# Kernel optimization log

Hardware: AMD Instinct MI355X
Metric: run time of the kernel (lower is better)

The kernel has to match this reference:

```python
import jax, jax.numpy as jnp
import numpy as np

B, C, D, W, H = 4, 256, 32, 32, 32  # img_dim = D, in_channels = C, model_num = 4


def setup_inputs() -> dict:
    key = jax.random.key(0)
    ks = jax.random.split(key, 8)
    s = 0.02
    inp = {
        "m1": jax.random.normal(ks[0], (B, C, D, W, H), jnp.float32),
        "m2": jax.random.normal(ks[1], (B, C, D, W, H), jnp.float32),
        "m3": jax.random.normal(ks[2], (B, C, D, W, H), jnp.float32),
        "m4": jax.random.normal(ks[3], (B, C, D, W, H), jnp.float32),
        # nn.Linear weights (torch convention: y = x @ W.T + b)
        "Wq": jax.random.normal(ks[4], (D, D), jnp.float32) * s,
        "bq": jnp.zeros((D,), jnp.float32),
        "Wk": jax.random.normal(ks[5], (D, D), jnp.float32) * s,
        "bk": jnp.zeros((D,), jnp.float32),
        # four 1x1x1 Conv3d kernels, squeezed to [model, out_c, in_c]
        "Wc": jax.random.normal(ks[6], (4, C, C), jnp.float32) * s,
        "bc": jnp.zeros((4, C), jnp.float32),
    }
    return inp


def reference(m1, m2, m3, m4, Wq, bq, Wk, bk, Wc, bc):
    d = m1.shape[2]
    # adaptive_avg_pool3d(x, (D,1,1)) == mean over W,H -> [B,C,D]; stack 4 modalities -> [B,C,4,D]
    pooled = jnp.stack([m.mean(axis=(3, 4)) for m in (m1, m2, m3, m4)], axis=2)
    q = jnp.einsum('bcd,ed->bce', pooled[:, :, 0], Wq) + bq          # [B,C,D]
    k = jnp.einsum('bcmd,ed->bcme', pooled, Wk) + bk                 # [B,C,4,D]
    # per-modality attention logits: q . k_m over D -> [B,C,4]
    a = jnp.einsum('bcd,bcmd->bcm', q, k) / jnp.sqrt(jnp.float32(d))
    a = jax.nn.softmax(a, axis=-1)                                   # [B,C,4]
    ms = jnp.stack([m1, m2, m3, m4], axis=0)                         # [4,B,C,D,W,H]
    # 1x1x1 Conv3d == channel-mixing GEMM per voxel
    conv = jnp.einsum('mbcdwh,moc->mbodwh', ms, Wc) + bc[:, None, :, None, None, None]
    # weighted sum of the 4 conv outputs by per-(B,C) attention weights
    out = jnp.einsum('bcm,mbcdwh->bcdwh', a, conv)                   # [B,C,D,W,H]
    return out
```

## Files before the change

### kernel.cpp

```cpp
#include <hip/hip_runtime.h>
#include <hip/hip_bf16.h>

#define NB 4
#define NC 256
#define ND 32
#define WH 1024
#define DWH 32768
#define KTOT 1024

typedef __attribute__((ext_vector_type(8))) short short8;
typedef __attribute__((ext_vector_type(4))) float f32x4;

static __device__ __forceinline__ unsigned short f32_to_bf16(float f) {
    unsigned u = __builtin_bit_cast(unsigned, f);
    u = u + 0x7fff + ((u >> 16) & 1);
    return (unsigned short)(u >> 16);
}

static __device__ __forceinline__ unsigned pack_bf16x2(float lo, float hi) {
    __hip_bfloat162 h = __float22bfloat162_rn(make_float2(lo, hi));
    unsigned u;
    __builtin_memcpy(&u, &h, 4);
    return u;
}

__global__ __launch_bounds__(256) void transpool_kernel(
    const float* __restrict__ i0, const float* __restrict__ i1,
    const float* __restrict__ i2, const float* __restrict__ i3,
    unsigned short* __restrict__ Bt, float* __restrict__ pooled)
{
    __shared__ float lds[64 * 132];
    int bid = blockIdx.x;
    int d  = bid & 31;
    int cb = (bid >> 5) & 3;
    int m  = (bid >> 7) & 3;
    int b  = bid >> 9;
    const float* base = (m == 0 ? i0 : m == 1 ? i1 : m == 2 ? i2 : i3)
                        + ((size_t)(b * NC + cb * 64)) * DWH + d * WH;
    int t  = threadIdx.x;
    int rl = t >> 3;
    int xo = t & 7;
    int xr = t >> 1;
    int ch = t & 1;

    float pc0 = 0.f, pc1 = 0.f;
    float4 v0[4], v1[4];

    #pragma unroll
    for (int j = 0; j < 4; ++j) {
        v0[j] = *(const float4*)(base + (size_t)rl * DWH + (xo + 8 * j) * 4);
        v1[j] = *(const float4*)(base + (size_t)(32 + rl) * DWH + (xo + 8 * j) * 4);
    }
    #pragma unroll
    for (int j = 0; j < 4; ++j) {
        pc0 += v0[j].x + v0[j].y + v0[j].z + v0[j].w;
        pc1 += v1[j].x + v1[j].y + v1[j].z + v1[j].w;
        *(float4*)&lds[rl * 132 + (xo + 8 * j) * 4]        = v0[j];
        *(float4*)&lds[(32 + rl) * 132 + (xo + 8 * j) * 4] = v1[j];
    }
    __syncthreads();

    unsigned short* tb0 = Bt + (((size_t)b * 256 + d * 8) * 16 + (m * 4 + cb)) * 8192;

    #pragma unroll 1
    for (int s = 0; s < 8; ++s) {
        if (s < 7) {
            const float* bs = base + (s + 1) * 128;
            #pragma unroll
            for (int j = 0; j < 4; ++j) {
                v0[j] = *(const float4*)(bs + (size_t)rl * DWH + (xo + 8 * j) * 4);
                v1[j] = *(const float4*)(bs + (size_t)(32 + rl) * DWH + (xo + 8 * j) * 4);
            }
        }
        {
            unsigned short* dst = tb0 + (size_t)s * 16 * 8192 + (size_t)xr * 64 + ch * 32;
            unsigned pk[16];
            #pragma unroll
            for (int i = 0; i < 16; ++i) {
                float f0 = lds[(ch * 32 + 2 * i) * 132 + xr];
                float f1 = lds[(ch * 32 + 2 * i + 1) * 132 + xr];
                pk[i] = pack_bf16x2(f0, f1);
            }
            #pragma unroll
            for (int u = 0; u < 4; ++u)
                *(uint4*)(dst + u * 8) =
                    (uint4){pk[4 * u], pk[4 * u + 1], pk[4 * u + 2], pk[4 * u + 3]};
        }
        __syncthreads();
        if (s < 7) {
            #pragma unroll
            for (int j = 0; j < 4; ++j) {
                pc0 += v0[j].x + v0[j].y + v0[j].z + v0[j].w;
                pc1 += v1[j].x + v1[j].y + v1[j].z + v1[j].w;
                *(float4*)&lds[rl * 132 + (xo + 8 * j) * 4]        = v0[j];
                *(float4*)&lds[(32 + rl) * 132 + (xo + 8 * j) * 4] = v1[j];
            }
            __syncthreads();
        }
    }

    pc0 += __shfl_down(pc0, 4, 64); pc1 += __shfl_down(pc1, 4, 64);
    pc0 += __shfl_down(pc0, 2, 64); pc1 += __shfl_down(pc1, 2, 64);
    pc0 += __shfl_down(pc0, 1, 64); pc1 += __shfl_down(pc1, 1, 64);
    if (xo == 0) {
        pooled[((size_t)b * NC + cb * 64 + rl) * 128 + m * 32 + d]      = pc0 * (1.0f / 1024.0f);
        pooled[((size_t)b * NC + cb * 64 + 32 + rl) * 128 + m * 32 + d] = pc1 * (1.0f / 1024.0f);
    }
}

__global__ __launch_bounds__(256) void pool_kernel(
    const float* __restrict__ i0, const float* __restrict__ i1,
    const float* __restrict__ i2, const float* __restrict__ i3,
    float* __restrict__ pooled)
{
    int bid = blockIdx.x;
    int m   = bid & 3;
    int bc  = bid >> 2;
    const float* src = (m == 0 ? i0 : m == 1 ? i1 : m == 2 ? i2 : i3)
                       + (size_t)bc * DWH;
    int t = threadIdx.x;
    int d   = t >> 3;
    int sub = t & 7;

    const float4* row = (const float4*)(src + (size_t)d * WH);
    float4 a0 = {0.f, 0.f, 0.f, 0.f}, a1 = {0.f, 0.f, 0.f, 0.f};
    #pragma unroll
    for (int j = 0; j < 16; ++j) {
        float4 u = row[sub + 8 * (2 * j)];
        float4 w = row[sub + 8 * (2 * j + 1)];
        a0.x += u.x; a0.y += u.y; a0.z += u.z; a0.w += u.w;
        a1.x += w.x; a1.y += w.y; a1.z += w.z; a1.w += w.w;
    }
    float s = (a0.x + a0.y) + (a0.z + a0.w) + (a1.x + a1.y) + (a1.z + a1.w);
    s += __shfl_down(s, 4, 64);
    s += __shfl_down(s, 2, 64);
    s += __shfl_down(s, 1, 64);
    if (sub == 0) pooled[bc * 128 + m * 32 + d] = s * (1.0f / 1024.0f);
}

__global__ __launch_bounds__(64) void attn_kernel(
    const float* __restrict__ pooled,
    const float* __restrict__ Wq, const float* __restrict__ bq,
    const float* __restrict__ Wk, const float* __restrict__ bk,
    const float* __restrict__ Wc, const float* __restrict__ bcv,
    unsigned short* __restrict__ Amat, float* __restrict__ beff)
{
    int bc_idx = blockIdx.x;
    int lane = threadIdx.x;
    int e = lane & 31;
    const float* P = pooled + bc_idx * 128;

    float q = 0.f, kv[4] = {0.f, 0.f, 0.f, 0.f};
    for (int d = 0; d < 32; ++d) {
        float pq = P[d];
        float wq = Wq[e * 32 + d], wk = Wk[e * 32 + d];
        q += pq * wq;
        #pragma unroll
        for (int m = 0; m < 4; ++m) kv[m] += P[m * 32 + d] * wk;
    }
    q += bq[e];
    #pragma unroll
    for (int m = 0; m < 4; ++m) kv[m] += bk[e];

    float lg[4];
    #pragma unroll
    for (int m = 0; m < 4; ++m) {
        float p = q * kv[m];
        #pragma unroll
        for (int off = 16; off; off >>= 1) p += __shfl_xor(p, off, 32);
        lg[m] = p * 0.17677669529663687f;
    }
    float mx = fmaxf(fmaxf(lg[0], lg[1]), fmaxf(lg[2], lg[3]));
    float ex[4], s = 0.f;
    #pragma unroll
    for (int m = 0; m < 4; ++m) { ex[m] = __expf(lg[m] - mx); s += ex[m]; }
    float a[4];
    #pragma unroll
    for (int m = 0; m < 4; ++m) a[m] = ex[m] / s;

    int c = bc_idx & 255;
    if (lane == 0) {
        float be = 0.f;
        #pragma unroll
        for (int m = 0; m < 4; ++m) be += a[m] * bcv[m * NC + c];
        beff[bc_idx] = be;
    }
    unsigned short* Arow = Amat + (size_t)bc_idx * KTOT;
    #pragma unroll
    for (int j = 0; j < 16; ++j) {
        int k = j * 64 + lane;
        int m = k >> 8, cin = k & 255;
        float v = a[m] * Wc[(m * NC + c) * NC + cin];
        Arow[k] = f32_to_bf16(v);
    }
}

#define BM 128
#define BN 128
#define BK 64

static __device__ __forceinline__ int swzA(int row, int chunk) {
    return row * 64 + ((chunk ^ (row & 7)) << 3);
}
static __device__ __forceinline__ int swzB(int row, int chunk) {
    return row * 64 + ((chunk ^ ((row >> 1) & 7)) << 3);
}

__global__ __launch_bounds__(256, 2) void gemm2_kernel(
    const unsigned short* __restrict__ Amat,
    const unsigned short* __restrict__ Bt,
    const float* __restrict__ beff,
    float* __restrict__ out)
{
    __shared__ __align__(16) short As[2 * BM * BK];
    __shared__ __align__(16) short Bs[2 * BN * BK];

    int raw = blockIdx.x;
    int sb  = (raw & 7) * 256 + (raw >> 3);
    int ot = sb & 1;
    int xt = (sb >> 1) & 255;
    int b  = sb >> 9;
    int o0 = ot * BM, x0 = xt * BN;

    int t = threadIdx.x;
    int wave = t >> 6, lane = t & 63;
    int wr = wave >> 1, wc = wave & 1;
    int lrow = lane & 15, lk = lane >> 4;
    int lr8 = lane >> 3;
    int aq  = (lane & 7) ^ lr8;

    const unsigned short* asrc = Amat + ((size_t)b * NC + o0) * KTOT
                                 + (size_t)(wave * 32 + lr8) * KTOT + aq * 8;
    const unsigned short* bsrc = Bt + ((size_t)b * 256 + xt) * 16 * 8192
                                 + (size_t)(wave * 32 + lr8) * 64 + aq * 8;

    f32x4 acc[4][4];
    #pragma unroll
    for (int mi = 0; mi < 4; ++mi)
        #pragma unroll
        for (int ni = 0; ni < 4; ++ni)
            acc[mi][ni] = (f32x4){0.f, 0.f, 0.f, 0.f};

    #pragma unroll
    for (int p = 0; p < 4; ++p)
        __builtin_amdgcn_global_load_lds(
            (const __attribute__((address_space(1))) unsigned int*)
                (asrc + (size_t)p * 8 * KTOT),
            (__attribute__((address_space(3))) unsigned int*)
                (As + (wave * 32 + p * 8) * 64), 16, 0, 0);
    #pragma unroll
    for (int p = 0; p < 4; ++p)
        __builtin_amdgcn_global_load_lds(
            (const __attribute__((address_space(1))) unsigned int*)
                (bsrc + (size_t)p * 8 * 64),
            (__attribute__((address_space(3))) unsigned int*)
                (Bs + (wave * 32 + p * 8) * 64), 16, 0, 0);
    __builtin_amdgcn_sched_barrier(0);

    #pragma unroll 1
    for (int it = 0; it < 16; ++it) {
        int ja = (it < 15) ? it + 1 : 15;
        int bo = ((it + 1) & 1) * (BM * BK);
        #pragma unroll
        for (int p = 0; p < 4; ++p)
            __builtin_amdgcn_global_load_lds(
                (const __attribute__((address_space(1))) unsigned int*)
                    (asrc + (size_t)p * 8 * KTOT + ja * BK),
                (__attribute__((address_space(3))) unsigned int*)
                    (As + bo + (wave * 32 + p * 8) * 64), 16, 0, 0);
        #pragma unroll
        for (int p = 0; p < 4; ++p)
            __builtin_amdgcn_global_load_lds(
                (const __attribute__((address_space(1))) unsigned int*)
                    (bsrc + (size_t)ja * 8192 + p * 8 * 64),
                (__attribute__((address_space(3))) unsigned int*)
                    (Bs + bo + (wave * 32 + p * 8) * 64), 16, 0, 0);
        __builtin_amdgcn_sched_barrier(0);

        asm volatile("s_waitcnt vmcnt(8)" ::: "memory");
        __builtin_amdgcn_s_barrier();
        __builtin_amdgcn_sched_barrier(0);

        const short* Acur = As + (it & 1) * (BM * BK);
        const short* Bcur = Bs + (it & 1) * (BM * BK);
        #pragma unroll
        for (int kk = 0; kk < 2; ++kk) {
            int q = kk * 4 + lk;
            short8 af[4], bf[4];
            #pragma unroll
            for (int mi = 0; mi < 4; ++mi)
                af[mi] = *(const short8*)(&Acur[swzA(wr * 64 + mi * 16 + lrow, q)]);
            #pragma unroll
            for (int ni = 0; ni < 4; ++ni)
                bf[ni] = *(const short8*)(&Bcur[swzA(wc * 64 + ni * 16 + lrow, q)]);
            __builtin_amdgcn_s_setprio(1);
            #pragma unroll
            for (int mi = 0; mi < 4; ++mi)
                #pragma unroll
                for (int ni = 0; ni < 4; ++ni)
                    acc[mi][ni] = __builtin_amdgcn_mfma_f32_16x16x32_bf16(
                        af[mi], bf[ni], acc[mi][ni], 0, 0, 0);
            __builtin_amdgcn_s_setprio(0);
        }
        __builtin_amdgcn_s_barrier();
        __builtin_amdgcn_sched_barrier(0);
    }

    const float* beff_b = beff + b * NC + o0;
    float* outb = out + ((size_t)b * NC + o0) * DWH + x0;
    #pragma unroll
    for (int mi = 0; mi < 4; ++mi) {
        #pragma unroll
        for (int r4 = 0; r4 < 4; ++r4) {
            int row = wr * 64 + mi * 16 + lk * 4 + r4;
            float bias = beff_b[row];
            float* orow = outb + (size_t)row * DWH;
            #pragma unroll
            for (int ni = 0; ni < 4; ++ni) {
                int col = wc * 64 + ni * 16 + lrow;
                orow[col] = acc[mi][ni][r4] + bias;
            }
        }
    }
}

__global__ __launch_bounds__(256, 3) void gemm_kernel(
    const float* __restrict__ i0, const float* __restrict__ i1,
    const float* __restrict__ i2, const float* __restrict__ i3,
    const unsigned short* __restrict__ Amat,
    const float* __restrict__ beff,
    float* __restrict__ out)
{
    __shared__ __align__(16) short As[2 * BM * BK];
    __shared__ __align__(16) short Bs[BN * BK];

    int raw = blockIdx.x;
    int sb  = (raw & 7) * 256 + (raw >> 3);
    int ot = sb & 1;
    int xt = (sb >> 1) & 255;
    int b  = sb >> 9;
    int o0 = ot * BM, x0 = xt * BN;

    const unsigned short* Ab = Amat + ((size_t)b * NC + o0) * KTOT;

    int t = threadIdx.x;
    int wave = t >> 6, lane = t & 63;
    int wr = wave >> 1, wc = wave & 1;
    int lrow = lane & 15, lk = lane >> 4;

    f32x4 acc[4][4];
    #pragma unroll
    for (int mi = 0; mi < 4; ++mi)
        #pragma unroll
        for (int ni = 0; ni < 4; ++ni)
            acc[mi][ni] = (f32x4){0.f, 0.f, 0.f, 0.f};

    int xq = t & 31;
    int kb = (t >> 5) * 8;

    int ar = wave * 32 + (lane >> 3);
    int aq = (lane & 7) ^ (lane >> 3);
    const unsigned short* asrc = Ab + (size_t)ar * KTOT + aq * 8;

    float4 v[8];

    {
        #pragma unroll
        for (int p = 0; p < 4; ++p)
            __builtin_amdgcn_global_load_lds(
                (const __attribute__((address_space(1))) unsigned int*)
                    (asrc + (size_t)p * 8 * KTOT),
                (__attribute__((address_space(3))) unsigned int*)
                    (As + (wave * 32 + p * 8) * 64), 16, 0, 0);
        const float* Bb = i0 + (size_t)b * NC * DWH + x0;
        #pragma unroll
        for (int j = 0; j < 8; ++j)
            v[j] = *(const float4*)(Bb + (size_t)(kb + j) * DWH + xq * 4);
    }

    #pragma unroll 1
    for (int it = 0; it < KTOT / BK; ++it) {
        const short* Acur = As + (it & 1) * (BM * BK);
        short* Anx = As + ((it + 1) & 1) * (BM * BK);

        __builtin_amdgcn_s_barrier();
        __builtin_amdgcn_sched_barrier(0);

        {
            int ja = (it + 1 < 16) ? it + 1 : 15;
            #pragma unroll
            for (int p = 0; p < 4; ++p)
                __builtin_amdgcn_global_load_lds(
                    (const __attribute__((address_space(1))) unsigned int*)
                        (asrc + (size_t)p * 8 * KTOT + ja * BK),
                    (__attribute__((address_space(3))) unsigned int*)
                        (Anx + (wave * 32 + p * 8) * 64), 16, 0, 0);
        }
        __builtin_amdgcn_sched_barrier(0);

        uint4 pk[4];
        #pragma unroll
        for (int i = 0; i < 4; ++i) {
            unsigned w[4];
            #pragma unroll
            for (int j = 0; j < 4; ++j)
                w[j] = pack_bf16x2(((const float*)&v[2 * j])[i],
                                   ((const float*)&v[2 * j + 1])[i]);
            pk[i] = (uint4){w[0], w[1], w[2], w[3]};
        }

        {
            int itn = (it < 15) ? it + 1 : 15;
            int m = itn >> 2, cbase = (itn & 3) * 64;
            const float* Bb = (m == 0 ? i0 : m == 1 ? i1 : m == 2 ? i2 : i3)
                              + ((size_t)b * NC + cbase) * DWH + x0;
            #pragma unroll
            for (int j = 0; j < 8; ++j)
                v[j] = *(const float4*)(Bb + (size_t)(kb + j) * DWH + xq * 4);
        }
        __builtin_amdgcn_sched_barrier(0);

        #pragma unroll
        for (int i = 0; i < 4; ++i)
            *(uint4*)(&Bs[swzB(xq * 4 + i, t >> 5)]) = pk[i];

        asm volatile("s_waitcnt vmcnt(12) lgkmcnt(0)" ::: "memory");
        __builtin_amdgcn_s_barrier();
        __builtin_amdgcn_sched_barrier(0);

        #pragma unroll
        for (int kk = 0; kk < 2; ++kk) {
            int q = kk * 4 + lk;
            short8 af[4], bf[4];
            #pragma unroll
            for (int mi = 0; mi < 4; ++mi)
                af[mi] = *(const short8*)(&Acur[swzA(wr * 64 + mi * 16 + lrow, q)]);
            #pragma unroll
            for (int ni = 0; ni < 4; ++ni)
                bf[ni] = *(const short8*)(&Bs[swzB(wc * 64 + ni * 16 + lrow, q)]);
            __builtin_amdgcn_s_setprio(1);
            #pragma unroll
            for (int mi = 0; mi < 4; ++mi)
                #pragma unroll
                for (int ni = 0; ni < 4; ++ni)
                    acc[mi][ni] = __builtin_amdgcn_mfma_f32_16x16x32_bf16(
                        af[mi], bf[ni], acc[mi][ni], 0, 0, 0);
            __builtin_amdgcn_s_setprio(0);
        }
    }

    const float* beff_b = beff + b * NC + o0;
    float* outb = out + ((size_t)b * NC + o0) * DWH + x0;
    #pragma unroll
    for (int mi = 0; mi < 4; ++mi) {
        #pragma unroll
        for (int r4 = 0; r4 < 4; ++r4) {
            int row = wr * 64 + mi * 16 + lk * 4 + r4;
            float bias = beff_b[row];
            float* orow = outb + (size_t)row * DWH;
            #pragma unroll
            for (int ni = 0; ni < 4; ++ni) {
                int col = wc * 64 + ni * 16 + lrow;
                orow[col] = acc[mi][ni][r4] + bias;
            }
        }
    }
}

extern "C" void kernel_launch(void* const* d_in, const int* in_sizes, int n_in,
                              void* d_out, int out_size, void* d_ws, size_t ws_size,
                              hipStream_t stream) {
    const float* m1 = (const float*)d_in[0];
    const float* m2 = (const float*)d_in[1];
    const float* m3 = (const float*)d_in[2];
    const float* m4 = (const float*)d_in[3];
    const float* Wq = (const float*)d_in[4];
    const float* bq = (const float*)d_in[5];
    const float* Wk = (const float*)d_in[6];
    const float* bk = (const float*)d_in[7];
    const float* Wc = (const float*)d_in[8];
    const float* bcv = (const float*)d_in[9];
    float* out = (float*)d_out;

    const size_t BT_BYTES = (size_t)NB * KTOT * DWH * 2;
    const size_t NEED = BT_BYTES + 524288 + 2097152 + 4096;

    if (ws_size >= NEED) {
        unsigned short* Btr   = (unsigned short*)d_ws;
        float* pooled         = (float*)((char*)d_ws + BT_BYTES);
        unsigned short* Amat  = (unsigned short*)((char*)d_ws + BT_BYTES + 524288);
        float* beff           = (float*)((char*)d_ws + BT_BYTES + 524288 + 2097152);

        transpool_kernel<<<2048, 256, 0, stream>>>(m1, m2, m3, m4, Btr, pooled);
        attn_kernel<<<NB * NC, 64, 0, stream>>>(pooled, Wq, bq, Wk, bk, Wc, bcv,
                                                Amat, beff);
        gemm2_kernel<<<2048, 256, 0, stream>>>(Amat, Btr, beff, out);
    } else {
        float* pooled        = (float*)d_ws;
        unsigned short* Amat = (unsigned short*)((char*)d_ws + 524288);
        float* beff          = (float*)((char*)d_ws + 524288 + 2097152);

        pool_kernel<<<NB * NC * 4, 256, 0, stream>>>(m1, m2, m3, m4, pooled);
        attn_kernel<<<NB * NC, 64, 0, stream>>>(pooled, Wq, bq, Wk, bk, Wc, bcv,
                                                Amat, beff);
        gemm_kernel<<<(NB) * (NC / BM) * (DWH / BN), 256, 0, stream>>>(
            m1, m2, m3, m4, Amat, beff, out);
    }
}
```

Measured before the change: 305.9 us.

## Double-buffer register loads and rework LDS transpose layout in transpool kernel

The transpose+pool kernel now keeps two register buffers of input tiles, so loads for step s+2 are in flight while step s is written out, instead of prefetching only one step ahead. The LDS row stride goes from 132 to 133 floats, and the store phase is remapped so each thread reads 8 consecutive channel rows and writes one 16-byte chunk per output row. Together these aim to hide global load latency and cut LDS bank conflicts. The cost is more registers per thread, which may lower occupancy, and scalar LDS writes where vector writes were used before.

Result: faster. 289.7 us (-5.3%).

```diff
diff --git a/kernel.cpp b/kernel.cpp
--- a/kernel.cpp
+++ b/kernel.cpp
@@ -24,12 +24,49 @@
     return u;
 }
 
+#define TP_LOAD(V, S)                                                         \
+  { const float* bs_ = base + (S) * 128;                                      \
+    _Pragma("unroll")                                                         \
+    for (int j_ = 0; j_ < 4; ++j_) {                                          \
+      V[j_]     = *(const float4*)(bs_ + (size_t)rl * DWH + (xo + 8 * j_) * 4);\
+      V[j_ + 4] = *(const float4*)(bs_ + (size_t)(32 + rl) * DWH + (xo + 8 * j_) * 4);\
+    } }
+
+#define TP_STAGE(V)                                                           \
+  { _Pragma("unroll")                                                         \
+    for (int j_ = 0; j_ < 4; ++j_) {                                          \
+      float4 u_ = V[j_], w_ = V[j_ + 4];                                      \
+      pc0 += u_.x + u_.y + u_.z + u_.w;                                       \
+      pc1 += w_.x + w_.y + w_.z + w_.w;                                       \
+      int xb_ = (xo + 8 * j_) * 4;                                            \
+      lds[rl * 133 + xb_ + 0] = u_.x;  lds[rl * 133 + xb_ + 1] = u_.y;        \
+      lds[rl * 133 + xb_ + 2] = u_.z;  lds[rl * 133 + xb_ + 3] = u_.w;        \
+      lds[(32 + rl) * 133 + xb_ + 0] = w_.x;  lds[(32 + rl) * 133 + xb_ + 1] = w_.y;\
+      lds[(32 + rl) * 133 + xb_ + 2] = w_.z;  lds[(32 + rl) * 133 + xb_ + 3] = w_.w;\
+    } }
+
+#define TP_STORE(S)                                                           \
+  { unsigned short* tile_ = tb0 + (size_t)(S) * 16 * 8192;                    \
+    _Pragma("unroll")                                                         \
+    for (int u_ = 0; u_ < 4; ++u_) {                                          \
+      int row_ = u_ * 32 + rl;                                                \
+      unsigned w0_ = pack_bf16x2(lds[(8 * xo + 0) * 133 + row_],              \
+                                 lds[(8 * xo + 1) * 133 + row_]);             \
+      unsigned w1_ = pack_bf16x2(lds[(8 * xo + 2) * 133 + row_],              \
+                                 lds[(8 * xo + 3) * 133 + row_]);             \
+      unsigned w2_ = pack_bf16x2(lds[(8 * xo + 4) * 133 + row_],              \
+                                 lds[(8 * xo + 5) * 133 + row_]);             \
+      unsigned w3_ = pack_bf16x2(lds[(8 * xo + 6) * 133 + row_],              \
+                                 lds[(8 * xo + 7) * 133 + row_]);             \
+      *(uint4*)(tile_ + (size_t)row_ * 64 + xo * 8) = (uint4){w0_, w1_, w2_, w3_};\
+    } }
+
 __global__ __launch_bounds__(256) void transpool_kernel(
     const float* __restrict__ i0, const float* __restrict__ i1,
     const float* __restrict__ i2, const float* __restrict__ i3,
     unsigned short* __restrict__ Bt, float* __restrict__ pooled)
 {
-    __shared__ float lds[64 * 132];
+    __shared__ float lds[64 * 133];
     int bid = blockIdx.x;
     int d  = bid & 31;
     int cb = (bid >> 5) & 3;
@@ -40,61 +77,30 @@
     int t  = threadIdx.x;
     int rl = t >> 3;
     int xo = t & 7;
-    int xr = t >> 1;
-    int ch = t & 1;
 
     float pc0 = 0.f, pc1 = 0.f;
-    float4 v0[4], v1[4];
-
-    #pragma unroll
-    for (int j = 0; j < 4; ++j) {
-        v0[j] = *(const float4*)(base + (size_t)rl * DWH + (xo + 8 * j) * 4);
-        v1[j] = *(const float4*)(base + (size_t)(32 + rl) * DWH + (xo + 8 * j) * 4);
-    }
-    #pragma unroll
-    for (int j = 0; j < 4; ++j) {
-        pc0 += v0[j].x + v0[j].y + v0[j].z + v0[j].w;
-        pc1 += v1[j].x + v1[j].y + v1[j].z + v1[j].w;
-        *(float4*)&lds[rl * 132 + (xo + 8 * j) * 4]        = v0[j];
-        *(float4*)&lds[(32 + rl) * 132 + (xo + 8 * j) * 4] = v1[j];
-    }
+    float4 va[8], vb[8];
+
+    unsigned short* tb0 = Bt + (((size_t)b * 256 + d * 8) * 16 + (m * 4 + cb)) * 8192;
+
+    TP_LOAD(va, 0);
+    TP_LOAD(vb, 1);
+    TP_STAGE(va);
     __syncthreads();
 
-    unsigned short* tb0 = Bt + (((size_t)b * 256 + d * 8) * 16 + (m * 4 + cb)) * 8192;
-
     #pragma unroll 1
-    for (int s = 0; s < 8; ++s) {
-        if (s < 7) {
-            const float* bs = base + (s + 1) * 128;
-            #pragma unroll
-            for (int j = 0; j < 4; ++j) {
-                v0[j] = *(const float4*)(bs + (size_t)rl * DWH + (xo + 8 * j) * 4);
-                v1[j] = *(const float4*)(bs + (size_t)(32 + rl) * DWH + (xo + 8 * j) * 4);
-            }
-        }
-        {
-            unsigned short* dst = tb0 + (size_t)s * 16 * 8192 + (size_t)xr * 64 + ch * 32;
-            unsigned pk[16];
-            #pragma unroll
-            for (int i = 0; i < 16; ++i) {
-                float f0 = lds[(ch * 32 + 2 * i) * 132 + xr];
-                float f1 = lds[(ch * 32 + 2 * i + 1) * 132 + xr];
-                pk[i] = pack_bf16x2(f0, f1);
-            }
-            #pragma unroll
-            for (int u = 0; u < 4; ++u)
-                *(uint4*)(dst + u * 8) =
-                    (uint4){pk[4 * u], pk[4 * u + 1], pk[4 * u + 2], pk[4 * u + 3]};
-        }
+    for (int s2 = 0; s2 < 4; ++s2) {
+        int s = 2 * s2;
+        if (s2 < 3) TP_LOAD(va, s + 2);
+        TP_STORE(s);
         __syncthreads();
-        if (s < 7) {
-            #pragma unroll
-            for (int j = 0; j < 4; ++j) {
-                pc0 += v0[j].x + v0[j].y + v0[j].z + v0[j].w;
-                pc1 += v1[j].x + v1[j].y + v1[j].z + v1[j].w;
-                *(float4*)&lds[rl * 132 + (xo + 8 * j) * 4]        = v0[j];
-                *(float4*)&lds[(32 + rl) * 132 + (xo + 8 * j) * 4] = v1[j];
-            }
+        TP_STAGE(vb);
+        __syncthreads();
+        if (s2 < 3) TP_LOAD(vb, s + 3);
+        TP_STORE(s + 1);
+        __syncthreads();
+        if (s2 < 3) {
+            TP_STAGE(va);
             __syncthreads();
         }
     }
```

## Split transpose-pool kernel into small 8-channel blocks with XCD-aware block remap

Applied to the files above, without the earlier changes.

The fused transpose-and-pool kernel is restructured so that each block handles 8 channels by one depth slice in a single pass. Previously each block covered 64 channels and looped over 8 staging rounds. The grid grows from 2048 to 16384 blocks, and block ids are remapped by stride 8, apparently to spread work across the chip's compute dies. Each thread now writes 16-byte bf16 chunks that hold 8 channels, and the pooled mean uses a wider shuffle reduction. This aims to raise parallelism and remove the loop's per-round synchronization, at the cost of narrower 16-byte output writes scattered across memory and more blocks to launch.

Result: slower. 514.7 us (+68.3%).

```diff
diff --git a/kernel.cpp b/kernel.cpp
--- a/kernel.cpp
+++ b/kernel.cpp
@@ -29,82 +29,69 @@
     const float* __restrict__ i2, const float* __restrict__ i3,
     unsigned short* __restrict__ Bt, float* __restrict__ pooled)
 {
-    __shared__ float lds[64 * 132];
-    int bid = blockIdx.x;
-    int d  = bid & 31;
-    int cb = (bid >> 5) & 3;
-    int m  = (bid >> 7) & 3;
-    int b  = bid >> 9;
+    __shared__ float lds[8 * 1024];
+    int raw = blockIdx.x;
+    int sb  = (raw & 7) * 2048 + (raw >> 3);
+    int d    = sb & 31;
+    int cb8  = (sb >> 5) & 31;
+    int m    = (sb >> 10) & 3;
+    int b    = sb >> 12;
     const float* base = (m == 0 ? i0 : m == 1 ? i1 : m == 2 ? i2 : i3)
-                        + ((size_t)(b * NC + cb * 64)) * DWH + d * WH;
-    int t  = threadIdx.x;
-    int rl = t >> 3;
-    int xo = t & 7;
-    int xr = t >> 1;
-    int ch = t & 1;
-
-    float pc0 = 0.f, pc1 = 0.f;
-    float4 v0[4], v1[4];
-
-    #pragma unroll
-    for (int j = 0; j < 4; ++j) {
-        v0[j] = *(const float4*)(base + (size_t)rl * DWH + (xo + 8 * j) * 4);
-        v1[j] = *(const float4*)(base + (size_t)(32 + rl) * DWH + (xo + 8 * j) * 4);
-    }
-    #pragma unroll
-    for (int j = 0; j < 4; ++j) {
-        pc0 += v0[j].x + v0[j].y + v0[j].z + v0[j].w;
-        pc1 += v1[j].x + v1[j].y + v1[j].z + v1[j].w;
-        *(float4*)&lds[rl * 132 + (xo + 8 * j) * 4]        = v0[j];
-        *(float4*)&lds[(32 + rl) * 132 + (xo + 8 * j) * 4] = v1[j];
-    }
+                        + ((size_t)(b * NC + cb8 * 8)) * DWH + d * WH;
+
+    int t = threadIdx.x;
+    int row    = t >> 5;
+    int lane32 = t & 31;
+
+    float4 v[8];
+    #pragma unroll
+    for (int j = 0; j < 8; ++j)
+        v[j] = *(const float4*)(base + (size_t)row * DWH + lane32 * 4 + j * 128);
+
+    float s = 0.f;
+    #pragma unroll
+    for (int j = 0; j < 8; ++j)
+        s += (v[j].x + v[j].y) + (v[j].z + v[j].w);
+
+    #pragma unroll
+    for (int j = 0; j < 8; ++j)
+        *(float4*)&lds[row * 1024 + lane32 * 4 + j * 128] = v[j];
     __syncthreads();
 
-    unsigned short* tb0 = Bt + (((size_t)b * 256 + d * 8) * 16 + (m * 4 + cb)) * 8192;
-
-    #pragma unroll 1
-    for (int s = 0; s < 8; ++s) {
-        if (s < 7) {
-            const float* bs = base + (s + 1) * 128;
-            #pragma unroll
-            for (int j = 0; j < 4; ++j) {
-                v0[j] = *(const float4*)(bs + (size_t)rl * DWH + (xo + 8 * j) * 4);
-                v1[j] = *(const float4*)(bs + (size_t)(32 + rl) * DWH + (xo + 8 * j) * 4);
-            }
-        }
-        {
-            unsigned short* dst = tb0 + (size_t)s * 16 * 8192 + (size_t)xr * 64 + ch * 32;
-            unsigned pk[16];
-            #pragma unroll
-            for (int i = 0; i < 16; ++i) {
-                float f0 = lds[(ch * 32 + 2 * i) * 132 + xr];
-                float f1 = lds[(ch * 32 + 2 * i + 1) * 132 + xr];
-                pk[i] = pack_bf16x2(f0, f1);
-            }
-            #pragma unroll
-            for (int u = 0; u < 4; ++u)
-                *(uint4*)(dst + u * 8) =
-                    (uint4){pk[4 * u], pk[4 * u + 1], pk[4 * u + 2], pk[4 * u + 3]};
-        }
-        __syncthreads();
-        if (s < 7) {
-            #pragma unroll
-            for (int j = 0; j < 4; ++j) {
-                pc0 += v0[j].x + v0[j].y + v0[j].z + v0[j].w;
-                pc1 += v1[j].x + v1[j].y + v1[j].z + v1[j].w;
-                *(float4*)&lds[rl * 132 + (xo + 8 * j) * 4]        = v0[j];
-                *(float4*)&lds[(32 + rl) * 132 + (xo + 8 * j) * 4] = v1[j];
-            }
-            __syncthreads();
-        }
-    }
-
-    pc0 += __shfl_down(pc0, 4, 64); pc1 += __shfl_down(pc1, 4, 64);
-    pc0 += __shfl_down(pc0, 2, 64); pc1 += __shfl_down(pc1, 2, 64);
-    pc0 += __shfl_down(pc0, 1, 64); pc1 += __shfl_down(pc1, 1, 64);
-    if (xo == 0) {
-        pooled[((size_t)b * NC + cb * 64 + rl) * 128 + m * 32 + d]      = pc0 * (1.0f / 1024.0f);
-        pooled[((size_t)b * NC + cb * 64 + 32 + rl) * 128 + m * 32 + d] = pc1 * (1.0f / 1024.0f);
+    float4 c0 = *(const float4*)&lds[0 * 1024 + 4 * t];
+    float4 c1 = *(const float4*)&lds[1 * 1024 + 4 * t];
+    float4 c2 = *(const float4*)&lds[2 * 1024 + 4 * t];
+    float4 c3 = *(const float4*)&lds[3 * 1024 + 4 * t];
+    float4 c4 = *(const float4*)&lds[4 * 1024 + 4 * t];
+    float4 c5 = *(const float4*)&lds[5 * 1024 + 4 * t];
+    float4 c6 = *(const float4*)&lds[6 * 1024 + 4 * t];
+    float4 c7 = *(const float4*)&lds[7 * 1024 + 4 * t];
+
+    unsigned short* tb0 = Bt + (((size_t)b * 256 + d * 8) * 16
+                                + (m * 4 + (cb8 >> 3))) * 8192
+                             + (cb8 & 7) * 8;
+    #pragma unroll
+    for (int xi = 0; xi < 4; ++xi) {
+        int x = 4 * t + xi;
+        const float* f0 = (const float*)&c0;  const float* f1 = (const float*)&c1;
+        const float* f2 = (const float*)&c2;  const float* f3 = (const float*)&c3;
+        const float* f4 = (const float*)&c4;  const float* f5 = (const float*)&c5;
+        const float* f6 = (const float*)&c6;  const float* f7 = (const float*)&c7;
+        uint4 pk = (uint4){pack_bf16x2(f0[xi], f1[xi]),
+                           pack_bf16x2(f2[xi], f3[xi]),
+                           pack_bf16x2(f4[xi], f5[xi]),
+                           pack_bf16x2(f6[xi], f7[xi])};
+        *(uint4*)(tb0 + (size_t)(x >> 7) * 16 * 8192 + (size_t)(x & 127) * 64) = pk;
+    }
+
+    s += __shfl_down(s, 16, 64);
+    s += __shfl_down(s, 8, 64);
+    s += __shfl_down(s, 4, 64);
+    s += __shfl_down(s, 2, 64);
+    s += __shfl_down(s, 1, 64);
+    if (lane32 == 0) {
+        int c = cb8 * 8 + row;
+        pooled[((size_t)b * NC + c) * 128 + m * 32 + d] = s * (1.0f / 1024.0f);
     }
 }
 
@@ -491,7 +478,7 @@
         unsigned short* Amat  = (unsigned short*)((char*)d_ws + BT_BYTES + 524288);
         float* beff           = (float*)((char*)d_ws + BT_BYTES + 524288 + 2097152);
 
-        transpool_kernel<<<2048, 256, 0, stream>>>(m1, m2, m3, m4, Btr, pooled);
+        transpool_kernel<<<16384, 256, 0, stream>>>(m1, m2, m3, m4, Btr, pooled);
         attn_kernel<<<NB * NC, 64, 0, stream>>>(pooled, Wq, bq, Wk, bk, Wc, bcv,
                                                 Amat, beff);
         gemm2_kernel<<<2048, 256, 0, stream>>>(Amat, Btr, beff, out);
```
